# Performance work log

Hardware: AMD Instinct MI355X
Metric: run time of the kernel (lower is better)

The kernel has to match this reference:

```python
import jax, jax.numpy as jnp
import numpy as np

B, CIN, COUT, H, W, K = 4, 3, 16, 256, 256, 5
PAD = K // 2  # replicate padding keeps spatial size


def _dilation_sum(x, w):
    """Learnable dilation, channel_merge_mode='sum'.
    x: (B,Cin,H,W), w: (Cout,Cin,K,K).
    out[b,o,i,j] = sum_c max_{di,dj} ( x_pad[b,c,i+di,j+dj] + w[o,c,di,dj] )
    """
    xp = jnp.pad(x, ((0, 0), (0, 0), (PAD, PAD), (PAD, PAD)), mode='edge')
    acc = jnp.full((x.shape[0], w.shape[0], x.shape[1], H, W), -jnp.inf, dtype=x.dtype)
    for di in range(K):  # fixed small kernel loop (unrolled), not a data-dim loop
        for dj in range(K):
            win = xp[:, :, di:di + H, dj:dj + W]                     # (B,Cin,H,W)
            cand = win[:, None] + w[None, :, :, di, dj][:, :, :, None, None]  # (B,Cout,Cin,H,W)
            acc = jnp.maximum(acc, cand)
    return acc.sum(axis=2)  # merge over input channels -> (B,Cout,H,W)


def _erosion_identity(y, w):
    """Learnable erosion, channel_merge_mode='identity' (each channel independent).
    y: (B,Cout,H,W), w: (Cout,K,K).
    out[b,o,i,j] = min_{di,dj} ( y_pad[b,o,i+di,j+dj] - w[o,di,dj] )
    """
    yp = jnp.pad(y, ((0, 0), (0, 0), (PAD, PAD), (PAD, PAD)), mode='edge')
    acc = jnp.full(y.shape, jnp.inf, dtype=y.dtype)
    for di in range(K):
        for dj in range(K):
            acc = jnp.minimum(acc, yp[:, :, di:di + H, dj:dj + W] - w[None, :, di, dj, None, None])
    return acc


def setup_inputs() -> dict:
    key = jax.random.key(0)
    k1, k2, k3 = jax.random.split(key, 3)
    x = jax.random.normal(k1, (B, CIN, H, W), dtype=jnp.float32)
    w_d = jax.random.normal(k2, (COUT, CIN, K, K), dtype=jnp.float32) * 0.05
    w_e = jax.random.normal(k3, (COUT, K, K), dtype=jnp.float32) * 0.05
    return {"x": x, "w_d": w_d, "w_e": w_e}


def reference(x, w_d, w_e):
    # Closing = dilation (max-plus, sum merge) followed by erosion (min-plus, identity merge)
    dilated = _dilation_sum(x, w_d)
    return _erosion_identity(dilated, w_e)
```

## Files before the change

kernel.cpp:

```cpp
#include <hip/hip_runtime.h>


typedef _Float16 h2 __attribute__((ext_vector_type(2)));

namespace {
constexpr int HH = 256, WW = 256, CI = 3;
constexpr int XS2 = 36;
constexpr int CH2 = 40 * XS2;
constexpr int DS2 = 36;
}

struct __align__(16) h2x4 { h2 a, b, c, d; };
struct __align__(8)  h2x2 { h2 a, b; };

__device__ __forceinline__ h2 pmax(h2 a, h2 b) { return __builtin_elementwise_max(a, b); }
__device__ __forceinline__ h2 pmin(h2 a, h2 b) { return __builtin_elementwise_min(a, b); }

__device__ __forceinline__ h2 shr1(h2 lo, h2 hi) {
    unsigned a = __builtin_bit_cast(unsigned, lo);
    unsigned b = __builtin_bit_cast(unsigned, hi);
    unsigned r = (a >> 16) | (b << 16);
    return __builtin_bit_cast(h2, r);
}

__device__ __forceinline__ void dtaps(h2& m0, h2& m1, h2& m2, h2& m3,
                                      const h2x4 A, const h2x2 B,
                                      h2 w0, h2 w1, h2 w2, h2 w3, h2 w4) {
    const h2 s0 = shr1(A.a, A.b), s1 = shr1(A.b, A.c), s2 = shr1(A.c, A.d),
             s3 = shr1(A.d, B.a), s4 = shr1(B.a, B.b);
    m0 = pmax(m0, pmax(pmax(A.a + w0, s0 + w1), pmax(A.b + w2, pmax(s1 + w3, A.c + w4))));
    m1 = pmax(m1, pmax(pmax(A.b + w0, s1 + w1), pmax(A.c + w2, pmax(s2 + w3, A.d + w4))));
    m2 = pmax(m2, pmax(pmax(A.c + w0, s2 + w1), pmax(A.d + w2, pmax(s3 + w3, B.a + w4))));
    m3 = pmax(m3, pmax(pmax(A.d + w0, s3 + w1), pmax(B.a + w2, pmax(s4 + w3, B.b + w4))));
}

__device__ __forceinline__ void etaps(h2& m0, h2& m1, h2& m2, h2& m3,
                                      const h2x4 A, const h2x2 B,
                                      h2 w0, h2 w1, h2 w2, h2 w3, h2 w4) {
    const h2 s0 = shr1(A.a, A.b), s1 = shr1(A.b, A.c), s2 = shr1(A.c, A.d),
             s3 = shr1(A.d, B.a), s4 = shr1(B.a, B.b);
    m0 = pmin(m0, pmin(pmin(A.a + w0, s0 + w1), pmin(A.b + w2, pmin(s1 + w3, A.c + w4))));
    m1 = pmin(m1, pmin(pmin(A.b + w0, s1 + w1), pmin(A.c + w2, pmin(s2 + w3, A.d + w4))));
    m2 = pmin(m2, pmin(pmin(A.c + w0, s2 + w1), pmin(A.d + w2, pmin(s3 + w3, B.a + w4))));
    m3 = pmin(m3, pmin(pmin(A.d + w0, s3 + w1), pmin(B.a + w2, pmin(s4 + w3, B.b + w4))));
}

__global__ __launch_bounds__(256, 4)
void closing_v8(const float* __restrict__ x, const float* __restrict__ wd,
                const float* __restrict__ we, float* __restrict__ out) {
    __shared__ __align__(16) h2 sx2[CI * CH2 + 8];
    __shared__ __align__(16) h2 sd2[36 * DS2];

    const int tid = threadIdx.x;
    const int bx = blockIdx.x, by = blockIdx.y, z = blockIdx.z;
    const int o = z & 15, b = z >> 4;
    const int i0 = by * 32, j0 = bx * 64;
    const float* xb = x + (size_t)b * (CI * HH * WW);

#pragma unroll
    for (int k = 0; k < 9; ++k) {
        const int idx = tid + (k << 8);
        if (idx < 2160) {
            const int c   = idx / 720;
            const int rem = idx - c * 720;
            const int r   = rem / 18;
            const int q   = rem - r * 18;
            const int gi  = min(max(i0 - 4 + r, 0), HH - 1);
            const int gj0 = j0 - 4 + (q << 2);
            const float* rowp = xb + c * (HH * WW) + (gi << 8);
            float4 v;
            if (gj0 < 0)        { const float t = rowp[0];      v = make_float4(t, t, t, t); }
            else if (gj0 > 252) { const float t = rowp[WW - 1]; v = make_float4(t, t, t, t); }
            else                  v = *(const float4*)(rowp + gj0);
            h2x2 hw;
            hw.a = h2{(_Float16)v.x, (_Float16)v.y};
            hw.b = h2{(_Float16)v.z, (_Float16)v.w};
            *(h2x2*)&sx2[c * CH2 + r * XS2 + (q << 1)] = hw;
        }
    }
    __syncthreads();

    for (int t = tid; t < 324; t += 256) {
        const int rr = t / 9, s = t - rr * 9;
        const int colh = s << 2;
        h2 acc0 = (h2)(_Float16)0.f, acc1 = acc0, acc2 = acc0, acc3 = acc0;
#pragma unroll
        for (int c = 0; c < CI; ++c) {
            const float* wr = wd + (o * CI + c) * 25;
            h2 m0 = (h2)(_Float16)-60000.f, m1 = m0, m2 = m0, m3 = m0;
            const int base = c * CH2 + rr * XS2 + colh;
#pragma unroll
            for (int r5 = 0; r5 < 5; ++r5) {
                const h2x4 A = *(const h2x4*)&sx2[base + r5 * XS2];
                const h2x2 B = *(const h2x2*)&sx2[base + r5 * XS2 + 4];
                const h2 w0 = (h2)(_Float16)wr[r5*5+0], w1 = (h2)(_Float16)wr[r5*5+1],
                         w2 = (h2)(_Float16)wr[r5*5+2], w3 = (h2)(_Float16)wr[r5*5+3],
                         w4 = (h2)(_Float16)wr[r5*5+4];
                dtaps(m0, m1, m2, m3, A, B, w0, w1, w2, w3, w4);
            }
            acc0 = acc0 + m0; acc1 = acc1 + m1; acc2 = acc2 + m2; acc3 = acc3 + m3;
        }
        if (bx == 0 && s == 0) acc0 = (h2)acc1.x;
        if (bx == 3 && s == 8) acc1 = (h2)acc0.y;
        bool store = true;
        if (by == 0 && rr < 2)  store = false;
        if (by == 7 && rr > 33) store = false;
        if (store) {
            const int db = rr * DS2 + colh;
            if (s < 8) { h2x4 w4v = {acc0, acc1, acc2, acc3}; *(h2x4*)&sd2[db] = w4v; }
            else       { h2x2 w2v = {acc0, acc1};             *(h2x2*)&sd2[db] = w2v; }
            if (by == 0 && rr == 2) {
#pragma unroll
                for (int pr = 0; pr < 2; ++pr) {
                    const int pb = pr * DS2 + colh;
                    if (s < 8) { h2x4 w4v = {acc0, acc1, acc2, acc3}; *(h2x4*)&sd2[pb] = w4v; }
                    else       { h2x2 w2v = {acc0, acc1};             *(h2x2*)&sd2[pb] = w2v; }
                }
            }
            if (by == 7 && rr == 33) {
#pragma unroll
                for (int pr = 34; pr < 36; ++pr) {
                    const int pb = pr * DS2 + colh;
                    if (s < 8) { h2x4 w4v = {acc0, acc1, acc2, acc3}; *(h2x4*)&sd2[pb] = w4v; }
                    else       { h2x2 w2v = {acc0, acc1};             *(h2x2*)&sd2[pb] = w2v; }
                }
            }
        }
    }
    __syncthreads();

    {
        const int r = tid >> 3, s = tid & 7;
        const float* ew = we + o * 25;
        h2 m0 = (h2)(_Float16)60000.f, m1 = m0, m2 = m0, m3 = m0;
        const int base = r * DS2 + (s << 2);
#pragma unroll
        for (int r5 = 0; r5 < 5; ++r5) {
            const h2x4 A = *(const h2x4*)&sd2[base + r5 * DS2];
            const h2x2 B = *(const h2x2*)&sd2[base + r5 * DS2 + 4];
            const h2 w0 = (h2)(_Float16)(-ew[r5*5+0]), w1 = (h2)(_Float16)(-ew[r5*5+1]),
                     w2 = (h2)(_Float16)(-ew[r5*5+2]), w3 = (h2)(_Float16)(-ew[r5*5+3]),
                     w4 = (h2)(_Float16)(-ew[r5*5+4]);
            etaps(m0, m1, m2, m3, A, B, w0, w1, w2, w3, w4);
        }
        float* op = &out[((size_t)z << 16) + ((size_t)(i0 + r) << 8) + j0 + (s << 3)];
        *(float4*)op       = make_float4((float)m0.x, (float)m0.y, (float)m1.x, (float)m1.y);
        *(float4*)(op + 4) = make_float4((float)m2.x, (float)m2.y, (float)m3.x, (float)m3.y);
    }
}

extern "C" void kernel_launch(void* const* d_in, const int* in_sizes, int n_in,
                              void* d_out, int out_size, void* d_ws, size_t ws_size,
                              hipStream_t stream) {
    const float* x  = (const float*)d_in[0];
    const float* wd = (const float*)d_in[1];
    const float* we = (const float*)d_in[2];
    float* out = (float*)d_out;

    dim3 grid(4, 8, 64);
    closing_v8<<<grid, dim3(256), 0, stream>>>(x, wd, we, out);
}
```

Before: 90.95 us.

## Enlarge fused tile to 60x60 with overlapping clamped tiles to cut halo recompute

Each block now produces a 60x60 output tile instead of 32x64, on a 5x5 grid whose last tile is clamped so it overlaps its neighbour. This lowers the fraction of dilation halo that is recomputed and the redundant input loads per output. Dilation threads now compute 8 half2 outputs each, and the erosion stage uses 300 work items of 12 outputs each. In exchange, per-thread register use and shared memory grow, and the overlapping tiles write some outputs twice.

```diff
diff --git a/kernel.cpp b/kernel.cpp
--- a/kernel.cpp
+++ b/kernel.cpp
@@ -6,12 +6,12 @@
 namespace {
 constexpr int HH = 256, WW = 256, CI = 3;
 constexpr int XS2 = 36;
-constexpr int CH2 = 40 * XS2;
+constexpr int CH2 = 68 * XS2;
 constexpr int DS2 = 36;
 }
 
-struct __align__(16) h2x4 { h2 a, b, c, d; };
-struct __align__(8)  h2x2 { h2 a, b; };
+struct __align__(16) H4  { h2 a, b, c, d; };
+struct __align__(8)  H2p { h2 a, b; };
 
 __device__ __forceinline__ h2 pmax(h2 a, h2 b) { return __builtin_elementwise_max(a, b); }
 __device__ __forceinline__ h2 pmin(h2 a, h2 b) { return __builtin_elementwise_min(a, b); }
@@ -19,52 +19,30 @@
 __device__ __forceinline__ h2 shr1(h2 lo, h2 hi) {
     unsigned a = __builtin_bit_cast(unsigned, lo);
     unsigned b = __builtin_bit_cast(unsigned, hi);
-    unsigned r = (a >> 16) | (b << 16);
-    return __builtin_bit_cast(h2, r);
-}
-
-__device__ __forceinline__ void dtaps(h2& m0, h2& m1, h2& m2, h2& m3,
-                                      const h2x4 A, const h2x2 B,
-                                      h2 w0, h2 w1, h2 w2, h2 w3, h2 w4) {
-    const h2 s0 = shr1(A.a, A.b), s1 = shr1(A.b, A.c), s2 = shr1(A.c, A.d),
-             s3 = shr1(A.d, B.a), s4 = shr1(B.a, B.b);
-    m0 = pmax(m0, pmax(pmax(A.a + w0, s0 + w1), pmax(A.b + w2, pmax(s1 + w3, A.c + w4))));
-    m1 = pmax(m1, pmax(pmax(A.b + w0, s1 + w1), pmax(A.c + w2, pmax(s2 + w3, A.d + w4))));
-    m2 = pmax(m2, pmax(pmax(A.c + w0, s2 + w1), pmax(A.d + w2, pmax(s3 + w3, B.a + w4))));
-    m3 = pmax(m3, pmax(pmax(A.d + w0, s3 + w1), pmax(B.a + w2, pmax(s4 + w3, B.b + w4))));
-}
-
-__device__ __forceinline__ void etaps(h2& m0, h2& m1, h2& m2, h2& m3,
-                                      const h2x4 A, const h2x2 B,
-                                      h2 w0, h2 w1, h2 w2, h2 w3, h2 w4) {
-    const h2 s0 = shr1(A.a, A.b), s1 = shr1(A.b, A.c), s2 = shr1(A.c, A.d),
-             s3 = shr1(A.d, B.a), s4 = shr1(B.a, B.b);
-    m0 = pmin(m0, pmin(pmin(A.a + w0, s0 + w1), pmin(A.b + w2, pmin(s1 + w3, A.c + w4))));
-    m1 = pmin(m1, pmin(pmin(A.b + w0, s1 + w1), pmin(A.c + w2, pmin(s2 + w3, A.d + w4))));
-    m2 = pmin(m2, pmin(pmin(A.c + w0, s2 + w1), pmin(A.d + w2, pmin(s3 + w3, B.a + w4))));
-    m3 = pmin(m3, pmin(pmin(A.d + w0, s3 + w1), pmin(B.a + w2, pmin(s4 + w3, B.b + w4))));
+    return __builtin_bit_cast(h2, (a >> 16) | (b << 16));
 }
 
 __global__ __launch_bounds__(256, 4)
-void closing_v8(const float* __restrict__ x, const float* __restrict__ wd,
+void closing_v9(const float* __restrict__ x, const float* __restrict__ wd,
                 const float* __restrict__ we, float* __restrict__ out) {
-    __shared__ __align__(16) h2 sx2[CI * CH2 + 8];
-    __shared__ __align__(16) h2 sd2[36 * DS2];
+    __shared__ __align__(16) h2 sx2[CI * CH2];
+    __shared__ __align__(16) h2 sd2[64 * DS2];
 
     const int tid = threadIdx.x;
     const int bx = blockIdx.x, by = blockIdx.y, z = blockIdx.z;
     const int o = z & 15, b = z >> 4;
-    const int i0 = by * 32, j0 = bx * 64;
+    const int i0 = min(by * 60, HH - 60);
+    const int j0 = min(bx * 60, WW - 60);
     const float* xb = x + (size_t)b * (CI * HH * WW);
 
 #pragma unroll
-    for (int k = 0; k < 9; ++k) {
+    for (int k = 0; k < 14; ++k) {
         const int idx = tid + (k << 8);
-        if (idx < 2160) {
-            const int c   = idx / 720;
-            const int rem = idx - c * 720;
-            const int r   = rem / 18;
-            const int q   = rem - r * 18;
+        if (idx < 3468) {
+            const int c   = idx / 1156;
+            const int rem = idx - c * 1156;
+            const int r   = rem / 17;
+            const int q   = rem - r * 17;
             const int gi  = min(max(i0 - 4 + r, 0), HH - 1);
             const int gj0 = j0 - 4 + (q << 2);
             const float* rowp = xb + c * (HH * WW) + (gi << 8);
@@ -72,80 +50,116 @@
             if (gj0 < 0)        { const float t = rowp[0];      v = make_float4(t, t, t, t); }
             else if (gj0 > 252) { const float t = rowp[WW - 1]; v = make_float4(t, t, t, t); }
             else                  v = *(const float4*)(rowp + gj0);
-            h2x2 hw;
+            H2p hw;
             hw.a = h2{(_Float16)v.x, (_Float16)v.y};
             hw.b = h2{(_Float16)v.z, (_Float16)v.w};
-            *(h2x2*)&sx2[c * CH2 + r * XS2 + (q << 1)] = hw;
+            *(H2p*)&sx2[c * CH2 + r * XS2 + (q << 1)] = hw;
         }
     }
     __syncthreads();
 
-    for (int t = tid; t < 324; t += 256) {
-        const int rr = t / 9, s = t - rr * 9;
-        const int colh = s << 2;
-        h2 acc0 = (h2)(_Float16)0.f, acc1 = acc0, acc2 = acc0, acc3 = acc0;
+    {
+        const int r = tid >> 2, s = tid & 3;
+        h2 acc[8];
+#pragma unroll
+        for (int k = 0; k < 8; ++k) acc[k] = (h2)(_Float16)0.f;
 #pragma unroll
         for (int c = 0; c < CI; ++c) {
             const float* wr = wd + (o * CI + c) * 25;
-            h2 m0 = (h2)(_Float16)-60000.f, m1 = m0, m2 = m0, m3 = m0;
-            const int base = c * CH2 + rr * XS2 + colh;
+            h2 m[8];
+#pragma unroll
+            for (int k = 0; k < 8; ++k) m[k] = (h2)(_Float16)-60000.f;
+            const int base = c * CH2 + r * XS2 + (s << 3);
 #pragma unroll
             for (int r5 = 0; r5 < 5; ++r5) {
-                const h2x4 A = *(const h2x4*)&sx2[base + r5 * XS2];
-                const h2x2 B = *(const h2x2*)&sx2[base + r5 * XS2 + 4];
-                const h2 w0 = (h2)(_Float16)wr[r5*5+0], w1 = (h2)(_Float16)wr[r5*5+1],
-                         w2 = (h2)(_Float16)wr[r5*5+2], w3 = (h2)(_Float16)wr[r5*5+3],
-                         w4 = (h2)(_Float16)wr[r5*5+4];
-                dtaps(m0, m1, m2, m3, A, B, w0, w1, w2, w3, w4);
+                const H4  A = *(const H4*)&sx2[base + r5 * XS2];
+                const H4  B = *(const H4*)&sx2[base + r5 * XS2 + 4];
+                const H2p C = *(const H2p*)&sx2[base + r5 * XS2 + 8];
+                const h2 h0=A.a,h1=A.b,h2_=A.c,h3=A.d,h4=B.a,h5=B.b,h6=B.c,h7=B.d,h8=C.a,h9=C.b;
+                const h2 t0=shr1(h0,h1),t1=shr1(h1,h2_),t2=shr1(h2_,h3),t3=shr1(h3,h4),
+                         t4=shr1(h4,h5),t5=shr1(h5,h6),t6=shr1(h6,h7),t7=shr1(h7,h8),
+                         t8=shr1(h8,h9);
+                const h2 w0=(h2)(_Float16)wr[r5*5+0], w1=(h2)(_Float16)wr[r5*5+1],
+                         w2=(h2)(_Float16)wr[r5*5+2], w3=(h2)(_Float16)wr[r5*5+3],
+                         w4=(h2)(_Float16)wr[r5*5+4];
+                m[0]=pmax(m[0],pmax(pmax(h0+w0,t0+w1),pmax(h1+w2,pmax(t1+w3,h2_+w4))));
+                m[1]=pmax(m[1],pmax(pmax(h1+w0,t1+w1),pmax(h2_+w2,pmax(t2+w3,h3+w4))));
+                m[2]=pmax(m[2],pmax(pmax(h2_+w0,t2+w1),pmax(h3+w2,pmax(t3+w3,h4+w4))));
+                m[3]=pmax(m[3],pmax(pmax(h3+w0,t3+w1),pmax(h4+w2,pmax(t4+w3,h5+w4))));
+                m[4]=pmax(m[4],pmax(pmax(h4+w0,t4+w1),pmax(h5+w2,pmax(t5+w3,h6+w4))));
+                m[5]=pmax(m[5],pmax(pmax(h5+w0,t5+w1),pmax(h6+w2,pmax(t6+w3,h7+w4))));
+                m[6]=pmax(m[6],pmax(pmax(h6+w0,t6+w1),pmax(h7+w2,pmax(t7+w3,h8+w4))));
+                m[7]=pmax(m[7],pmax(pmax(h7+w0,t7+w1),pmax(h8+w2,pmax(t8+w3,h9+w4))));
             }
-            acc0 = acc0 + m0; acc1 = acc1 + m1; acc2 = acc2 + m2; acc3 = acc3 + m3;
+#pragma unroll
+            for (int k = 0; k < 8; ++k) acc[k] = acc[k] + m[k];
         }
-        if (bx == 0 && s == 0) acc0 = (h2)acc1.x;
-        if (bx == 3 && s == 8) acc1 = (h2)acc0.y;
-        bool store = true;
-        if (by == 0 && rr < 2)  store = false;
-        if (by == 7 && rr > 33) store = false;
-        if (store) {
-            const int db = rr * DS2 + colh;
-            if (s < 8) { h2x4 w4v = {acc0, acc1, acc2, acc3}; *(h2x4*)&sd2[db] = w4v; }
-            else       { h2x2 w2v = {acc0, acc1};             *(h2x2*)&sd2[db] = w2v; }
-            if (by == 0 && rr == 2) {
+        if (j0 == 0        && s == 0) acc[0] = (h2)acc[1].x;
+        if (j0 == WW - 60  && s == 3) acc[7] = (h2)acc[6].y;
+        const bool top = (i0 == 0), bot = (i0 == HH - 60);
+        const bool skip = (top && r < 2) || (bot && r > 61);
+        if (!skip) {
+            const int db = r * DS2 + (s << 3);
 #pragma unroll
-                for (int pr = 0; pr < 2; ++pr) {
-                    const int pb = pr * DS2 + colh;
-                    if (s < 8) { h2x4 w4v = {acc0, acc1, acc2, acc3}; *(h2x4*)&sd2[pb] = w4v; }
-                    else       { h2x2 w2v = {acc0, acc1};             *(h2x2*)&sd2[pb] = w2v; }
-                }
+            for (int k = 0; k < 4; ++k) { H2p w2v = {acc[2*k], acc[2*k+1]};
+                                          *(H2p*)&sd2[db + (k << 1)] = w2v; }
+            if (top && r == 2) {
+#pragma unroll
+                for (int pr = 0; pr < 2; ++pr)
+#pragma unroll
+                    for (int k = 0; k < 4; ++k) { H2p w2v = {acc[2*k], acc[2*k+1]};
+                                                  *(H2p*)&sd2[pr * DS2 + (s << 3) + (k << 1)] = w2v; }
             }
-            if (by == 7 && rr == 33) {
+            if (bot && r == 61) {
 #pragma unroll
-                for (int pr = 34; pr < 36; ++pr) {
-                    const int pb = pr * DS2 + colh;
-                    if (s < 8) { h2x4 w4v = {acc0, acc1, acc2, acc3}; *(h2x4*)&sd2[pb] = w4v; }
-                    else       { h2x2 w2v = {acc0, acc1};             *(h2x2*)&sd2[pb] = w2v; }
-                }
+                for (int pr = 62; pr < 64; ++pr)
+#pragma unroll
+                    for (int k = 0; k < 4; ++k) { H2p w2v = {acc[2*k], acc[2*k+1]};
+                                                  *(H2p*)&sd2[pr * DS2 + (s << 3) + (k << 1)] = w2v; }
             }
         }
     }
     __syncthreads();
 
     {
-        const int r = tid >> 3, s = tid & 7;
         const float* ew = we + o * 25;
-        h2 m0 = (h2)(_Float16)60000.f, m1 = m0, m2 = m0, m3 = m0;
-        const int base = r * DS2 + (s << 2);
 #pragma unroll
-        for (int r5 = 0; r5 < 5; ++r5) {
-            const h2x4 A = *(const h2x4*)&sd2[base + r5 * DS2];
-            const h2x2 B = *(const h2x2*)&sd2[base + r5 * DS2 + 4];
-            const h2 w0 = (h2)(_Float16)(-ew[r5*5+0]), w1 = (h2)(_Float16)(-ew[r5*5+1]),
-                     w2 = (h2)(_Float16)(-ew[r5*5+2]), w3 = (h2)(_Float16)(-ew[r5*5+3]),
-                     w4 = (h2)(_Float16)(-ew[r5*5+4]);
-            etaps(m0, m1, m2, m3, A, B, w0, w1, w2, w3, w4);
+        for (int tt = 0; tt < 2; ++tt) {
+            const int t = tid + tt * 256;
+            if (t < 300) {
+                const int r = t / 5, s = t - r * 5;
+                const int eb = r * DS2 + 6 * s;
+                h2 n[6];
+#pragma unroll
+                for (int k = 0; k < 6; ++k) n[k] = (h2)(_Float16)60000.f;
+#pragma unroll
+                for (int r5 = 0; r5 < 5; ++r5) {
+                    const H2p q0 = *(const H2p*)&sd2[eb + r5 * DS2];
+                    const H2p q1 = *(const H2p*)&sd2[eb + r5 * DS2 + 2];
+                    const H2p q2 = *(const H2p*)&sd2[eb + r5 * DS2 + 4];
+                    const H2p q3 = *(const H2p*)&sd2[eb + r5 * DS2 + 6];
+                    const h2 e0=q0.a,e1=q0.b,e2=q1.a,e3=q1.b,e4=q2.a,e5=q2.b,e6=q3.a,e7=q3.b;
+                    const h2 t0=shr1(e0,e1),t1=shr1(e1,e2),t2=shr1(e2,e3),t3=shr1(e3,e4),
+                             t4=shr1(e4,e5),t5=shr1(e5,e6),t6=shr1(e6,e7);
+                    const h2 w0=(h2)(_Float16)(-ew[r5*5+0]), w1=(h2)(_Float16)(-ew[r5*5+1]),
+                             w2=(h2)(_Float16)(-ew[r5*5+2]), w3=(h2)(_Float16)(-ew[r5*5+3]),
+                             w4=(h2)(_Float16)(-ew[r5*5+4]);
+                    n[0]=pmin(n[0],pmin(pmin(e0+w0,t0+w1),pmin(e1+w2,pmin(t1+w3,e2+w4))));
+                    n[1]=pmin(n[1],pmin(pmin(e1+w0,t1+w1),pmin(e2+w2,pmin(t2+w3,e3+w4))));
+                    n[2]=pmin(n[2],pmin(pmin(e2+w0,t2+w1),pmin(e3+w2,pmin(t3+w3,e4+w4))));
+                    n[3]=pmin(n[3],pmin(pmin(e3+w0,t3+w1),pmin(e4+w2,pmin(t4+w3,e5+w4))));
+                    n[4]=pmin(n[4],pmin(pmin(e4+w0,t4+w1),pmin(e5+w2,pmin(t5+w3,e6+w4))));
+                    n[5]=pmin(n[5],pmin(pmin(e5+w0,t5+w1),pmin(e6+w2,pmin(t6+w3,e7+w4))));
+                }
+                float* op = &out[((size_t)z << 16) + ((size_t)(i0 + r) << 8) + j0 + 12 * s];
+                *(float4*)op       = make_float4((float)n[0].x, (float)n[0].y,
+                                                 (float)n[1].x, (float)n[1].y);
+                *(float4*)(op + 4) = make_float4((float)n[2].x, (float)n[2].y,
+                                                 (float)n[3].x, (float)n[3].y);
+                *(float4*)(op + 8) = make_float4((float)n[4].x, (float)n[4].y,
+                                                 (float)n[5].x, (float)n[5].y);
+            }
         }
-        float* op = &out[((size_t)z << 16) + ((size_t)(i0 + r) << 8) + j0 + (s << 3)];
-        *(float4*)op       = make_float4((float)m0.x, (float)m0.y, (float)m1.x, (float)m1.y);
-        *(float4*)(op + 4) = make_float4((float)m2.x, (float)m2.y, (float)m3.x, (float)m3.y);
     }
 }
 
@@ -157,6 +171,6 @@
     const float* we = (const float*)d_in[2];
     float* out = (float*)d_out;
 
-    dim3 grid(4, 8, 64);
-    closing_v8<<<grid, dim3(256), 0, stream>>>(x, wd, we, out);
+    dim3 grid(5, 5, 64);
+    closing_v9<<<grid, dim3(256), 0, stream>>>(x, wd, we, out);
 }
```

Result: slower. 230.7 us (+153.7%).
